# Optimization experiments

Hardware: AMD Instinct MI355X
Metric: run time of the kernel (lower is better)

The kernel has to match this reference:

```python
import jax, jax.numpy as jnp
import numpy as np

B, S, H = 1, 2048, 4096
NH, NKV, HD = 32, 8, 128
MAX_POS, ROPE_THETA = 4096, 10000.0


def setup_inputs() -> dict:
    key = jax.random.key(0)
    ks = jax.random.split(key, 6)
    hidden_states = jax.random.normal(ks[0], (B, S, H), dtype=jnp.float32)
    # additive causal mask (0 on/below diagonal, large negative above)
    causal = jnp.tril(jnp.ones((S, S), dtype=bool))
    attention_mask = jnp.where(causal, 0.0, -1e9).astype(jnp.float32)[None, None]
    position_ids = jnp.broadcast_to(jnp.arange(S, dtype=jnp.int32)[None, :], (B, S))
    sc = 0.02
    Wq = jax.random.normal(ks[1], (H, NH * HD), dtype=jnp.float32) * sc
    Wk = jax.random.normal(ks[2], (H, NKV * HD), dtype=jnp.float32) * sc
    Wv = jax.random.normal(ks[3], (H, NKV * HD), dtype=jnp.float32) * sc
    Wo = jax.random.normal(ks[4], (NH * HD, H), dtype=jnp.float32) * sc
    return {"hidden_states": hidden_states, "attention_mask": attention_mask,
            "position_ids": position_ids, "Wq": Wq, "Wk": Wk, "Wv": Wv, "Wo": Wo}


def _rotate_half(x):
    x1, x2 = x[..., : x.shape[-1] // 2], x[..., x.shape[-1] // 2 :]
    return jnp.concatenate((-x2, x1), axis=-1)


def _rope_tables(seq_len, dtype):
    inv_freq = 1.0 / (ROPE_THETA ** (jnp.arange(0, HD, 2, dtype=jnp.float32) / HD))
    t = jnp.arange(seq_len, dtype=jnp.float32)
    freqs = jnp.einsum("i,j->ij", t, inv_freq)        # [S, HD/2]
    emb = jnp.concatenate((freqs, freqs), axis=-1)     # [S, HD]
    return jnp.cos(emb).astype(dtype), jnp.sin(emb).astype(dtype)


def reference(hidden_states, attention_mask, position_ids, Wq, Wk, Wv, Wo):
    bsz, q_len, _ = hidden_states.shape
    # projections -> [b, h, s, d]
    q = (hidden_states @ Wq).reshape(bsz, q_len, NH, HD).swapaxes(1, 2)
    k = (hidden_states @ Wk).reshape(bsz, q_len, NKV, HD).swapaxes(1, 2)
    v = (hidden_states @ Wv).reshape(bsz, q_len, NKV, HD).swapaxes(1, 2)
    # rotary embedding
    cos, sin = _rope_tables(q_len, hidden_states.dtype)
    cos = jnp.take(cos, position_ids, axis=0)[:, None]  # [b,1,s,d]
    sin = jnp.take(sin, position_ids, axis=0)[:, None]
    q = q * cos + _rotate_half(q) * sin
    k = k * cos + _rotate_half(k) * sin
    # GQA: repeat kv heads
    n_rep = NH // NKV
    k = jnp.repeat(k, n_rep, axis=1)
    v = jnp.repeat(v, n_rep, axis=1)
    # attention
    scores = jnp.einsum("bhqd,bhkd->bhqk", q, k) / jnp.sqrt(jnp.float32(HD)).astype(q.dtype)
    scores = scores + attention_mask
    attn = jax.nn.softmax(scores, axis=-1)
    out = jnp.einsum("bhqk,bhkd->bhqd", attn, v)
    out = out.swapaxes(1, 2).reshape(bsz, q_len, NH * HD)
    return out @ Wo
```

## Files before the change

### kernel.cpp

```cpp
#include <hip/hip_runtime.h>

typedef unsigned short u16;
typedef __attribute__((ext_vector_type(8))) __bf16 bf16x8;
typedef __attribute__((ext_vector_type(8))) unsigned short u16x8;
typedef __attribute__((ext_vector_type(4))) float f32x4;

#define AS1 __attribute__((address_space(1)))
#define AS3 __attribute__((address_space(3)))

__device__ __forceinline__ void load_lds16(const void* g, void* l) {
  __builtin_amdgcn_global_load_lds((const AS1 unsigned int*)g,
                                   (AS3 unsigned int*)l, 16, 0, 0);
}

__device__ __forceinline__ float bf2f(u16 u) {
  unsigned int x = ((unsigned int)u) << 16;
  return __builtin_bit_cast(float, x);
}
__device__ __forceinline__ u16 f2bf(float f) {
  unsigned int x = __builtin_bit_cast(unsigned int, f);
  x += 0x7fffu + ((x >> 16) & 1u);
  return (u16)(x >> 16);
}
__device__ __forceinline__ bf16x8 cvt8(const float* p) {
  f32x4 a = *(const f32x4*)p;
  f32x4 b = *(const f32x4*)(p + 4);
  u16x8 r;
#pragma unroll
  for (int j = 0; j < 4; ++j) { r[j] = f2bf(a[j]); r[4 + j] = f2bf(b[j]); }
  return __builtin_bit_cast(bf16x8, r);
}

__global__ __launch_bounds__(256) void cvt_bf16_kernel(const float* __restrict__ in,
                                                       u16* __restrict__ out) {
  const int i = (blockIdx.x * 256 + threadIdx.x) * 8;
  *(bf16x8*)&out[i] = cvt8(in + i);
}

__global__ __launch_bounds__(256) void transpose_w(const float* __restrict__ in,
                                                   u16* __restrict__ out,
                                                   int R, int C, int col0) {
  __shared__ u16 tile[32][33];
  const int tx = threadIdx.x & 31, ty = threadIdx.x >> 5;
  const int c0 = blockIdx.x * 32, r0 = blockIdx.y * 32;
#pragma unroll
  for (int j = ty; j < 32; j += 8)
    tile[j][tx] = f2bf(in[(size_t)(r0 + j) * C + col0 + c0 + tx]);
  __syncthreads();
#pragma unroll
  for (int j = ty; j < 32; j += 8)
    out[(size_t)(c0 + j) * R + r0 + tx] = tile[tx][j];
}

__global__ __launch_bounds__(256) void gemm_kv(const u16* __restrict__ A,
                                               const u16* __restrict__ Bt,
                                               u16* __restrict__ Kb,
                                               u16* __restrict__ VTb) {
  const int K = 4096;
  __shared__ __align__(16) u16 As[128 * 32];
  __shared__ __align__(16) u16 Bs[128 * 32];
  const int tid = threadIdx.x, lane = tid & 63, w = tid >> 6;
  const int quad = lane >> 4, c16 = lane & 15;
  const int rw = lane >> 2, c4 = lane & 3;
  const int bm = blockIdx.x * 128, bn = blockIdx.y * 128;
  const int wm = (w >> 1) * 64, wn = (w & 1) * 64;

  f32x4 acc[4][4] = {};

  const u16* Ag0 = A + (size_t)(bm + w * 16 + rw) * K + c4 * 8;
  const u16* Ag1 = Ag0 + (size_t)64 * K;
  const u16* Bg0 = Bt + (size_t)(bn + w * 16 + rw) * K + c4 * 8;
  const u16* Bg1 = Bg0 + (size_t)64 * K;
  u16* As0 = &As[(w * 16) * 32];
  u16* As1 = &As[(64 + w * 16) * 32];
  u16* Bs0 = &Bs[(w * 16) * 32];
  u16* Bs1 = &Bs[(64 + w * 16) * 32];

  for (int k0 = 0; k0 < K; k0 += 32) {
    load_lds16(Ag0 + k0, As0);
    load_lds16(Ag1 + k0, As1);
    load_lds16(Bg0 + k0, Bs0);
    load_lds16(Bg1 + k0, Bs1);
    __syncthreads();
    bf16x8 a[4], b[4];
#pragma unroll
    for (int mt = 0; mt < 4; ++mt)
      a[mt] = *(const bf16x8*)&As[(wm + mt * 16 + c16) * 32 + quad * 8];
#pragma unroll
    for (int nt = 0; nt < 4; ++nt)
      b[nt] = *(const bf16x8*)&Bs[(wn + nt * 16 + c16) * 32 + quad * 8];
#pragma unroll
    for (int mt = 0; mt < 4; ++mt)
#pragma unroll
      for (int nt = 0; nt < 4; ++nt)
        acc[mt][nt] = __builtin_amdgcn_mfma_f32_16x16x32_bf16(a[mt], b[nt], acc[mt][nt], 0, 0, 0);
    __syncthreads();
  }
#pragma unroll
  for (int mt = 0; mt < 4; ++mt)
#pragma unroll
    for (int nt = 0; nt < 4; ++nt)
#pragma unroll
      for (int r = 0; r < 4; ++r) {
        const int row = bm + wm + mt * 16 + quad * 4 + r;
        const int col = bn + wn + nt * 16 + c16;
        if (bn < 1024)
          Kb[(size_t)row * 1024 + col] = f2bf(acc[mt][nt][r]);
        else
          VTb[(size_t)(col - 1024) * 2048 + row] = f2bf(acc[mt][nt][r]);
      }
}

__device__ __forceinline__ void stage_tile2(const u16* Ag, const u16* Bg,
                                            u16* Asb, u16* Bsb, int w, int K,
                                            int k0) {
#pragma unroll
  for (int j = 0; j < 2; ++j)
    load_lds16(Ag + (size_t)j * 64 * K + k0, Asb + j * 4096 + w * 512);
#pragma unroll
  for (int j = 0; j < 4; ++j)
    load_lds16(Bg + (size_t)j * 64 * K + k0, Bsb + j * 4096 + w * 512);
}

template <int OF32>
__global__ __launch_bounds__(512, 2) void gemm2(const u16* __restrict__ A,
                                                const u16* __restrict__ Bt,
                                                void* __restrict__ Cv,
                                                int K, int ldC) {
  __shared__ __align__(16) u16 As[3][128 * 64];
  __shared__ __align__(16) u16 Bs[3][256 * 64];
  const int tid = threadIdx.x, lane = tid & 63, w = tid >> 6;
  const int quad = lane >> 4, c16 = lane & 15;
  const int bm = blockIdx.x * 128, bn = blockIdx.y * 256;
  const int wm = (w >> 2) * 64, wn = (w & 3) * 64;

  const int l3 = lane >> 3, l7 = lane & 7;
  const int ss = l7 ^ l3;
  const u16* Ag = A + (size_t)(bm + w * 8 + l3) * K + ss * 8;
  const u16* Bg = Bt + (size_t)(bn + w * 8 + l3) * K + ss * 8;
  const int sx = (c16 & 7) << 4;

  f32x4 acc[4][4] = {};
  const int NT = K >> 6;

  stage_tile2(Ag, Bg, As[0], Bs[0], w, K, 0);
  stage_tile2(Ag, Bg, As[1], Bs[1], w, K, 64);
  int bc = 0;
  for (int kt = 0; kt < NT; ++kt) {
    __syncthreads();
    const int bp = bc + 2 >= 3 ? bc - 1 : bc + 2;
    if (kt + 2 < NT) stage_tile2(Ag, Bg, As[bp], Bs[bp], w, K, (kt + 2) << 6);

    const u16* Ab = As[bc];
    const u16* Bb = Bs[bc];
    bf16x8 a[4][2], b[4][2];
#pragma unroll
    for (int mt = 0; mt < 4; ++mt)
#pragma unroll
      for (int kc = 0; kc < 2; ++kc) {
        const int row = wm + mt * 16 + c16;
        a[mt][kc] = *(const bf16x8*)&Ab[(row * 128 + ((((kc * 4 + quad) << 4)) ^ sx)) >> 1];
      }
#pragma unroll
    for (int nt = 0; nt < 4; ++nt)
#pragma unroll
      for (int kc = 0; kc < 2; ++kc) {
        const int row = wn + nt * 16 + c16;
        b[nt][kc] = *(const bf16x8*)&Bb[(row * 128 + ((((kc * 4 + quad) << 4)) ^ sx)) >> 1];
      }
#pragma unroll
    for (int kc = 0; kc < 2; ++kc)
#pragma unroll
      for (int mt = 0; mt < 4; ++mt)
#pragma unroll
        for (int nt = 0; nt < 4; ++nt)
          acc[mt][nt] = __builtin_amdgcn_mfma_f32_16x16x32_bf16(a[mt][kc], b[nt][kc], acc[mt][nt], 0, 0, 0);
    bc = bc == 2 ? 0 : bc + 1;
  }
#pragma unroll
  for (int mt = 0; mt < 4; ++mt)
#pragma unroll
    for (int nt = 0; nt < 4; ++nt)
#pragma unroll
      for (int r = 0; r < 4; ++r) {
        const int row = bm + wm + mt * 16 + quad * 4 + r;
        const int col = bn + wn + nt * 16 + c16;
        if (OF32)
          ((float*)Cv)[(size_t)row * ldC + col] = acc[mt][nt][r];
        else
          ((u16*)Cv)[(size_t)row * ldC + col] = f2bf(acc[mt][nt][r]);
      }
}

__global__ void rope_kernel(u16* __restrict__ buf, const int* __restrict__ pos,
                            int log2nh, float oscale) {
  const int t = blockIdx.x * 256 + threadIdx.x;
  const int i = t & 63;
  const int h = (t >> 6) & ((1 << log2nh) - 1);
  const int s = t >> (6 + log2nh);
  const int nh = 1 << log2nh;
  const float p = (float)pos[s];
  const float invf = exp2f((float)i * -0.20762051915861040f);
  const float ang = p * invf;
  const float cn = cosf(ang), sn = sinf(ang);
  const size_t i1 = (size_t)s * (nh * 128) + h * 128 + i;
  const size_t i2 = i1 + 64;
  const float x1 = bf2f(buf[i1]), x2 = bf2f(buf[i2]);
  buf[i1] = f2bf((x1 * cn - x2 * sn) * oscale);
  buf[i2] = f2bf((x2 * cn + x1 * sn) * oscale);
}

__global__ __launch_bounds__(256, 2) void flash_kernel(const u16* __restrict__ Q,
                                                       const u16* __restrict__ K,
                                                       const u16* __restrict__ VT,
                                                       u16* __restrict__ O) {
  __shared__ __align__(16) u16 Ks[64 * 128];
  __shared__ __align__(16) u16 Vts[128 * 64];
  __shared__ __align__(16) u16 Ps[4][16 * 72];
  const int h = blockIdx.x, kvh = h >> 2;
  const int qb = 31 - blockIdx.y;
  const int tid = threadIdx.x, lane = tid & 63, w = tid >> 6;
  const int quad = lane >> 4, c16 = lane & 15;
  const int rw = lane >> 2, c4 = lane & 3;
  const int sw = (rw & 7) << 3;
  const int sr = (c16 & 7) << 3;

  bf16x8 aq[4];
#pragma unroll
  for (int kc = 0; kc < 4; ++kc)
    aq[kc] = *(const bf16x8*)&Q[(size_t)(qb * 64 + w * 16 + c16) * 4096 + h * 128 + kc * 32 + quad * 8];

  f32x4 acc_o[8] = {};
  float m_run[4], l_run[4];
#pragma unroll
  for (int r = 0; r < 4; ++r) { m_run[r] = -1e30f; l_run[r] = 0.f; }

  bf16x8 kc_[4], vc_[4];
#pragma unroll
  for (int p = 0; p < 4; ++p) {
    kc_[p] = *(const bf16x8*)&K[(size_t)(w * 16 + rw) * 1024 + kvh * 128 + p * 32 + c4 * 8];
    const int d = (p & 1) * 64 + w * 16 + rw;
    vc_[p] = *(const bf16x8*)&VT[(size_t)(kvh * 128 + d) * 2048 + (p >> 1) * 32 + c4 * 8];
  }

  for (int t = 0; t <= qb; ++t) {
    __syncthreads();
    const int key = w * 16 + rw;
#pragma unroll
    for (int p = 0; p < 4; ++p) {
      *(bf16x8*)&Ks[key * 128 + ((p * 32 + c4 * 8) ^ sw)] = kc_[p];
      const int d = (p & 1) * 64 + w * 16 + rw;
      *(bf16x8*)&Vts[d * 64 + ((((p >> 1) * 32 + c4 * 8)) ^ ((d & 7) << 3))] = vc_[p];
    }
    __syncthreads();
    if (t < qb) {
#pragma unroll
      for (int p = 0; p < 4; ++p) {
        kc_[p] = *(const bf16x8*)&K[(size_t)((t + 1) * 64 + w * 16 + rw) * 1024 + kvh * 128 + p * 32 + c4 * 8];
        const int d = (p & 1) * 64 + w * 16 + rw;
        vc_[p] = *(const bf16x8*)&VT[(size_t)(kvh * 128 + d) * 2048 + (t + 1) * 64 + (p >> 1) * 32 + c4 * 8];
      }
    }

    f32x4 sacc[4];
    __builtin_amdgcn_s_setprio(1);
#pragma unroll
    for (int nt = 0; nt < 4; ++nt) {
      f32x4 s = {0.f, 0.f, 0.f, 0.f};
#pragma unroll
      for (int kc = 0; kc < 4; ++kc) {
        bf16x8 bk = *(const bf16x8*)&Ks[(nt * 16 + c16) * 128 + ((kc * 32 + quad * 8) ^ sr)];
        s = __builtin_amdgcn_mfma_f32_16x16x32_bf16(aq[kc], bk, s, 0, 0, 0);
      }
      sacc[nt] = s;
    }
    __builtin_amdgcn_s_setprio(0);
    if (t == qb) {
#pragma unroll
      for (int nt = 0; nt < 4; ++nt)
#pragma unroll
        for (int r = 0; r < 4; ++r)
          if (nt * 16 + c16 > w * 16 + quad * 4 + r) sacc[nt][r] = -1e30f;
    }
    float al[4];
#pragma unroll
    for (int r = 0; r < 4; ++r) {
      float mx = fmaxf(fmaxf(sacc[0][r], sacc[1][r]), fmaxf(sacc[2][r], sacc[3][r]));
#pragma unroll
      for (int off = 1; off < 16; off <<= 1) mx = fmaxf(mx, __shfl_xor(mx, off));
      const float nm = fmaxf(m_run[r], mx);
      al[r] = __expf(m_run[r] - nm);
      m_run[r] = nm;
      float sum = 0.f;
#pragma unroll
      for (int nt = 0; nt < 4; ++nt) {
        const float pv = __expf(sacc[nt][r] - nm);
        sacc[nt][r] = pv;
        sum += pv;
      }
#pragma unroll
      for (int off = 1; off < 16; off <<= 1) sum += __shfl_xor(sum, off);
      l_run[r] = l_run[r] * al[r] + sum;
    }
#pragma unroll
    for (int dt = 0; dt < 8; ++dt)
#pragma unroll
      for (int r = 0; r < 4; ++r) acc_o[dt][r] *= al[r];
#pragma unroll
    for (int nt = 0; nt < 4; ++nt)
#pragma unroll
      for (int r = 0; r < 4; ++r)
        Ps[w][(quad * 4 + r) * 72 + nt * 16 + c16] = f2bf(sacc[nt][r]);
    asm volatile("s_waitcnt lgkmcnt(0)" ::: "memory");
    bf16x8 ap[2];
#pragma unroll
    for (int kc = 0; kc < 2; ++kc)
      ap[kc] = *(const bf16x8*)&Ps[w][c16 * 72 + kc * 32 + quad * 8];
    __builtin_amdgcn_s_setprio(1);
#pragma unroll
    for (int dt = 0; dt < 8; ++dt)
#pragma unroll
      for (int kc = 0; kc < 2; ++kc) {
        bf16x8 bv = *(const bf16x8*)&Vts[(dt * 16 + c16) * 64 + ((kc * 32 + quad * 8) ^ sr)];
        acc_o[dt] = __builtin_amdgcn_mfma_f32_16x16x32_bf16(ap[kc], bv, acc_o[dt], 0, 0, 0);
      }
    __builtin_amdgcn_s_setprio(0);
  }
#pragma unroll
  for (int r = 0; r < 4; ++r) {
    const float inv = 1.0f / l_run[r];
    const int row = qb * 64 + w * 16 + quad * 4 + r;
#pragma unroll
    for (int dt = 0; dt < 8; ++dt)
      O[(size_t)row * 4096 + h * 128 + dt * 16 + c16] = f2bf(acc_o[dt][r] * inv);
  }
}

extern "C" void kernel_launch(void* const* d_in, const int* in_sizes, int n_in,
                              void* d_out, int out_size, void* d_ws, size_t ws_size,
                              hipStream_t stream) {
  const float* X  = (const float*)d_in[0];
  const int* pos  = (const int*)d_in[2];
  const float* Wq = (const float*)d_in[3];
  const float* Wk = (const float*)d_in[4];
  const float* Wv = (const float*)d_in[5];
  const float* Wo = (const float*)d_in[6];
  float* out = (float*)d_out;

  const int NP = (ws_size >= (size_t)50331648) ? 4096 : 2048;
  char* ws = (char*)d_ws;
  u16* WT  = (u16*)ws;
  u16* Att = (u16*)(ws + (NP == 4096 ? 33554432 : 16777216));
  u16* Xb  = Att;
  u16* Qb  = (u16*)d_out;
  u16* Kb  = (u16*)((char*)d_out + 16777216);
  u16* VTb = (u16*)((char*)d_out + 20971520);

  const dim3 b256(256), b512(512);

  cvt_bf16_kernel<<<dim3(4096), b256, 0, stream>>>(X, Xb);

  for (int p = 0; p < 4096; p += NP) {
    transpose_w<<<dim3(NP / 32, 128), b256, 0, stream>>>(Wq, WT, 4096, 4096, p);
    gemm2<0><<<dim3(16, NP / 256), b512, 0, stream>>>(Xb, WT, Qb + p, 4096, 4096);
  }
  transpose_w<<<dim3(32, 128), b256, 0, stream>>>(Wk, WT, 4096, 1024, 0);
  transpose_w<<<dim3(32, 128), b256, 0, stream>>>(Wv, WT + (size_t)1024 * 4096, 4096, 1024, 0);
  gemm_kv<<<dim3(16, 16), b256, 0, stream>>>(Xb, WT, Kb, VTb);

  rope_kernel<<<dim3(2048 * 32 * 64 / 256), b256, 0, stream>>>(Qb, pos, 5, 0.08838834764831845f);
  rope_kernel<<<dim3(2048 * 8 * 64 / 256),  b256, 0, stream>>>(Kb, pos, 3, 1.0f);

  flash_kernel<<<dim3(32, 32), b256, 0, stream>>>(Qb, Kb, VTb, Att);

  for (int p = 0; p < 4096; p += NP) {
    transpose_w<<<dim3(NP / 32, 128), b256, 0, stream>>>(Wo, WT, 4096, 4096, p);
    gemm2<1><<<dim3(16, NP / 256), b512, 0, stream>>>(Att, WT, out + p, 4096, 4096);
  }
}
```

Measured before the change: 598.9 us.

## Use fine-grained vmcnt waits in gemm2, reuse it for KV projection, repad P tile

The gemm2 loop replaces __syncthreads with s_waitcnt vmcnt(6) plus a raw barrier, so the tile prefetched two steps ahead can stay in flight across the barrier. It also raises wave priority around the MFMA block. The separate single-buffered gemm_kv kernel is removed and the KV projection now runs through a new MODE 2 of the triple-buffered gemm2. In the flash kernel the P scratch row pitch changes from 72 to 68 with two 8-byte reads, to change the LDS bank pattern. The vmcnt count assumes exactly six outstanding loads per stage, which makes the synchronisation fragile if the staging code changes.

```diff
diff --git a/kernel.cpp b/kernel.cpp
--- a/kernel.cpp
+++ b/kernel.cpp
@@ -2,7 +2,9 @@
 
 typedef unsigned short u16;
 typedef __attribute__((ext_vector_type(8))) __bf16 bf16x8;
+typedef __attribute__((ext_vector_type(4))) __bf16 bf16x4;
 typedef __attribute__((ext_vector_type(8))) unsigned short u16x8;
+typedef __attribute__((ext_vector_type(4))) unsigned short u16x4;
 typedef __attribute__((ext_vector_type(4))) float f32x4;
 
 #define AS1 __attribute__((address_space(1)))
@@ -52,65 +54,6 @@
     out[(size_t)(c0 + j) * R + r0 + tx] = tile[tx][j];
 }
 
-__global__ __launch_bounds__(256) void gemm_kv(const u16* __restrict__ A,
-                                               const u16* __restrict__ Bt,
-                                               u16* __restrict__ Kb,
-                                               u16* __restrict__ VTb) {
-  const int K = 4096;
-  __shared__ __align__(16) u16 As[128 * 32];
-  __shared__ __align__(16) u16 Bs[128 * 32];
-  const int tid = threadIdx.x, lane = tid & 63, w = tid >> 6;
-  const int quad = lane >> 4, c16 = lane & 15;
-  const int rw = lane >> 2, c4 = lane & 3;
-  const int bm = blockIdx.x * 128, bn = blockIdx.y * 128;
-  const int wm = (w >> 1) * 64, wn = (w & 1) * 64;
-
-  f32x4 acc[4][4] = {};
-
-  const u16* Ag0 = A + (size_t)(bm + w * 16 + rw) * K + c4 * 8;
-  const u16* Ag1 = Ag0 + (size_t)64 * K;
-  const u16* Bg0 = Bt + (size_t)(bn + w * 16 + rw) * K + c4 * 8;
-  const u16* Bg1 = Bg0 + (size_t)64 * K;
-  u16* As0 = &As[(w * 16) * 32];
-  u16* As1 = &As[(64 + w * 16) * 32];
-  u16* Bs0 = &Bs[(w * 16) * 32];
-  u16* Bs1 = &Bs[(64 + w * 16) * 32];
-
-  for (int k0 = 0; k0 < K; k0 += 32) {
-    load_lds16(Ag0 + k0, As0);
-    load_lds16(Ag1 + k0, As1);
-    load_lds16(Bg0 + k0, Bs0);
-    load_lds16(Bg1 + k0, Bs1);
-    __syncthreads();
-    bf16x8 a[4], b[4];
-#pragma unroll
-    for (int mt = 0; mt < 4; ++mt)
-      a[mt] = *(const bf16x8*)&As[(wm + mt * 16 + c16) * 32 + quad * 8];
-#pragma unroll
-    for (int nt = 0; nt < 4; ++nt)
-      b[nt] = *(const bf16x8*)&Bs[(wn + nt * 16 + c16) * 32 + quad * 8];
-#pragma unroll
-    for (int mt = 0; mt < 4; ++mt)
-#pragma unroll
-      for (int nt = 0; nt < 4; ++nt)
-        acc[mt][nt] = __builtin_amdgcn_mfma_f32_16x16x32_bf16(a[mt], b[nt], acc[mt][nt], 0, 0, 0);
-    __syncthreads();
-  }
-#pragma unroll
-  for (int mt = 0; mt < 4; ++mt)
-#pragma unroll
-    for (int nt = 0; nt < 4; ++nt)
-#pragma unroll
-      for (int r = 0; r < 4; ++r) {
-        const int row = bm + wm + mt * 16 + quad * 4 + r;
-        const int col = bn + wn + nt * 16 + c16;
-        if (bn < 1024)
-          Kb[(size_t)row * 1024 + col] = f2bf(acc[mt][nt][r]);
-        else
-          VTb[(size_t)(col - 1024) * 2048 + row] = f2bf(acc[mt][nt][r]);
-      }
-}
-
 __device__ __forceinline__ void stage_tile2(const u16* Ag, const u16* Bg,
                                             u16* Asb, u16* Bsb, int w, int K,
                                             int k0) {
@@ -122,10 +65,11 @@
     load_lds16(Bg + (size_t)j * 64 * K + k0, Bsb + j * 4096 + w * 512);
 }
 
-template <int OF32>
+template <int MODE>
 __global__ __launch_bounds__(512, 2) void gemm2(const u16* __restrict__ A,
                                                 const u16* __restrict__ Bt,
                                                 void* __restrict__ Cv,
+                                                u16* __restrict__ C2,
                                                 int K, int ldC) {
   __shared__ __align__(16) u16 As[3][128 * 64];
   __shared__ __align__(16) u16 Bs[3][256 * 64];
@@ -147,7 +91,12 @@
   stage_tile2(Ag, Bg, As[1], Bs[1], w, K, 64);
   int bc = 0;
   for (int kt = 0; kt < NT; ++kt) {
-    __syncthreads();
+    if (kt < NT - 1)
+      asm volatile("s_waitcnt vmcnt(6)" ::: "memory");
+    else
+      asm volatile("s_waitcnt vmcnt(0)" ::: "memory");
+    __builtin_amdgcn_s_barrier();
+    asm volatile("" ::: "memory");
     const int bp = bc + 2 >= 3 ? bc - 1 : bc + 2;
     if (kt + 2 < NT) stage_tile2(Ag, Bg, As[bp], Bs[bp], w, K, (kt + 2) << 6);
 
@@ -168,6 +117,7 @@
         const int row = wn + nt * 16 + c16;
         b[nt][kc] = *(const bf16x8*)&Bb[(row * 128 + ((((kc * 4 + quad) << 4)) ^ sx)) >> 1];
       }
+    __builtin_amdgcn_s_setprio(1);
 #pragma unroll
     for (int kc = 0; kc < 2; ++kc)
 #pragma unroll
@@ -175,6 +125,7 @@
 #pragma unroll
         for (int nt = 0; nt < 4; ++nt)
           acc[mt][nt] = __builtin_amdgcn_mfma_f32_16x16x32_bf16(a[mt][kc], b[nt][kc], acc[mt][nt], 0, 0, 0);
+    __builtin_amdgcn_s_setprio(0);
     bc = bc == 2 ? 0 : bc + 1;
   }
 #pragma unroll
@@ -185,10 +136,16 @@
       for (int r = 0; r < 4; ++r) {
         const int row = bm + wm + mt * 16 + quad * 4 + r;
         const int col = bn + wn + nt * 16 + c16;
-        if (OF32)
+        if (MODE == 1)
           ((float*)Cv)[(size_t)row * ldC + col] = acc[mt][nt][r];
-        else
+        else if (MODE == 0)
           ((u16*)Cv)[(size_t)row * ldC + col] = f2bf(acc[mt][nt][r]);
+        else {
+          if (bn < 1024)
+            ((u16*)Cv)[(size_t)row * 1024 + col] = f2bf(acc[mt][nt][r]);
+          else
+            C2[(size_t)(col - 1024) * 2048 + row] = f2bf(acc[mt][nt][r]);
+        }
       }
 }
 
@@ -216,7 +173,7 @@
                                                        u16* __restrict__ O) {
   __shared__ __align__(16) u16 Ks[64 * 128];
   __shared__ __align__(16) u16 Vts[128 * 64];
-  __shared__ __align__(16) u16 Ps[4][16 * 72];
+  __shared__ __align__(16) u16 Ps[4][16 * 68];
   const int h = blockIdx.x, kvh = h >> 2;
   const int qb = 31 - blockIdx.y;
   const int tid = threadIdx.x, lane = tid & 63, w = tid >> 6;
@@ -310,12 +267,19 @@
     for (int nt = 0; nt < 4; ++nt)
 #pragma unroll
       for (int r = 0; r < 4; ++r)
-        Ps[w][(quad * 4 + r) * 72 + nt * 16 + c16] = f2bf(sacc[nt][r]);
+        Ps[w][(quad * 4 + r) * 68 + nt * 16 + c16] = f2bf(sacc[nt][r]);
     asm volatile("s_waitcnt lgkmcnt(0)" ::: "memory");
     bf16x8 ap[2];
 #pragma unroll
-    for (int kc = 0; kc < 2; ++kc)
-      ap[kc] = *(const bf16x8*)&Ps[w][c16 * 72 + kc * 32 + quad * 8];
+    for (int kc = 0; kc < 2; ++kc) {
+      const u16* pp = &Ps[w][c16 * 68 + kc * 32 + quad * 8];
+      bf16x4 lo = *(const bf16x4*)pp;
+      bf16x4 hi = *(const bf16x4*)(pp + 4);
+      bf16x8 apv;
+#pragma unroll
+      for (int j = 0; j < 4; ++j) { apv[j] = lo[j]; apv[4 + j] = hi[j]; }
+      ap[kc] = apv;
+    }
     __builtin_amdgcn_s_setprio(1);
 #pragma unroll
     for (int dt = 0; dt < 8; ++dt)
@@ -362,11 +326,11 @@
 
   for (int p = 0; p < 4096; p += NP) {
     transpose_w<<<dim3(NP / 32, 128), b256, 0, stream>>>(Wq, WT, 4096, 4096, p);
-    gemm2<0><<<dim3(16, NP / 256), b512, 0, stream>>>(Xb, WT, Qb + p, 4096, 4096);
+    gemm2<0><<<dim3(16, NP / 256), b512, 0, stream>>>(Xb, WT, Qb + p, nullptr, 4096, 4096);
   }
   transpose_w<<<dim3(32, 128), b256, 0, stream>>>(Wk, WT, 4096, 1024, 0);
   transpose_w<<<dim3(32, 128), b256, 0, stream>>>(Wv, WT + (size_t)1024 * 4096, 4096, 1024, 0);
-  gemm_kv<<<dim3(16, 16), b256, 0, stream>>>(Xb, WT, Kb, VTb);
+  gemm2<2><<<dim3(16, 8), b512, 0, stream>>>(Xb, WT, Kb, VTb, 4096, 0);
 
   rope_kernel<<<dim3(2048 * 32 * 64 / 256), b256, 0, stream>>>(Qb, pos, 5, 0.08838834764831845f);
   rope_kernel<<<dim3(2048 * 8 * 64 / 256),  b256, 0, stream>>>(Kb, pos, 3, 1.0f);
@@ -375,6 +339,6 @@
 
   for (int p = 0; p < 4096; p += NP) {
     transpose_w<<<dim3(NP / 32, 128), b256, 0, stream>>>(Wo, WT, 4096, 4096, p);
-    gemm2<1><<<dim3(16, NP / 256), b512, 0, stream>>>(Att, WT, out + p, 4096, 4096);
-  }
-}
+    gemm2<1><<<dim3(16, NP / 256), b512, 0, stream>>>(Att, WT, out + p, nullptr, 4096, 4096);
+  }
+}
```

After: 608.6 us. Within noise of the previous version (+1.6%).
